# Performance work log

Measured on AMD Instinct MI355X. Metric: run time of the kernel, lower is better.

The kernel has to match this reference:

```python
import jax, jax.numpy as jnp
import numpy as np

H, D = 20, 64  # n_head, head_dim (n_state = 1280)


def setup_inputs() -> dict:
    key = jax.random.key(0)
    ks = jax.random.split(key, 14)
    B, S, N, R = 2, 1500, 1280, 32
    s = 0.05  # keep activations/scores numerically tame
    return {
        "x":   jax.random.normal(ks[0], (B, S, N), jnp.float32),
        "Wq1": jax.random.normal(ks[1], (R, N), jnp.float32) * s,
        "Wq2": jax.random.normal(ks[2], (N, R), jnp.float32) * s,
        "bq":  jax.random.normal(ks[3], (N,), jnp.float32) * s,
        "Wk1": jax.random.normal(ks[4], (R, N), jnp.float32) * s,
        "Wk2": jax.random.normal(ks[5], (N, R), jnp.float32) * s,
        "bk":  jax.random.normal(ks[6], (N,), jnp.float32) * s,
        "Wv1": jax.random.normal(ks[7], (R, N), jnp.float32) * s,
        "Wv2": jax.random.normal(ks[8], (N, R), jnp.float32) * s,
        "bv":  jax.random.normal(ks[9], (N,), jnp.float32) * s,
        "Wo1": jax.random.normal(ks[10], (R, N), jnp.float32) * s,
        "Wo2": jax.random.normal(ks[11], (N, R), jnp.float32) * s,
        "bo":  jax.random.normal(ks[12], (N,), jnp.float32) * s,
    }


def reference(x, Wq1, Wq2, bq, Wk1, Wk2, bk, Wv1, Wv2, bv, Wo1, Wo2, bo):
    B, S, N = x.shape
    # rank-r projections (the only full-size GEMMs over x)
    q1 = x @ Wq1.T  # (B,S,rq)
    k1 = x @ Wk1.T  # (B,S,rk)
    v1 = x @ Wv1.T  # (B,S,rv)
    # per-head factors, matching prepare_custom_kernel()
    Wq2h = Wq2.reshape(H, D, -1).transpose(0, 2, 1)  # (H,rq,D)
    Wk2h = Wk2.reshape(H, D, -1)                     # (H,D,rk)
    Wv2h = Wv2.reshape(H, D, -1).transpose(0, 2, 1)  # (H,rv,D)
    Wm = Wq2h @ Wk2h                                  # (H,rq,rk)
    bqh = bq.reshape(H, 1, D)                         # (H,1,D)
    bkh = bk.reshape(H, 1, D).transpose(0, 2, 1)      # (H,D,1)
    b1 = (Wq2h @ bkh)[:, :, 0]                        # (H,rq)
    b2 = (bqh @ Wk2h)[:, 0, :]                        # (H,rk)
    b3 = (bqh @ bkh)[:, 0, 0]                         # (H,)
    # merged low-rank attention scores: (q1 Wq2 + bq)(Wk2^T k1^T + bk)
    scores = jnp.einsum('bir,hrt,bjt->bhij', q1, Wm, k1)
    scores = scores + jnp.einsum('bir,hr->bhi', q1, b1)[:, :, :, None]
    scores = scores + jnp.einsum('bjt,ht->bhj', k1, b2)[:, :, None, :]
    scores = scores + b3[None, :, None, None]
    attn = jax.nn.softmax(scores * (D ** -0.5), axis=-1)  # SDPA default scale
    Vh = jnp.einsum('bjr,hrd->bhjd', v1, Wv2h)            # (B,H,S,D)
    a = jnp.einsum('bhij,bhjd->bhid', attn, Vh)           # (B,H,S,D)
    wv = a.transpose(0, 2, 1, 3).reshape(B, S, H * D) + bv
    # out projection (also low-rank)
    return (wv @ Wo1.T) @ Wo2.T + bo
```

## Files before the change

### kernel.cpp

```cpp
#include <hip/hip_runtime.h>
#include <math.h>

#define Bb 2
#define Ss 1500
#define SP 1536
#define Nn 1280
#define Hh 20
#define Rr 32
#define NT 24

#define LOG2E 1.44269504088896f

typedef __attribute__((ext_vector_type(8))) short short8;
typedef __attribute__((ext_vector_type(4))) float f32x4;
typedef unsigned short ushort_t;

__device__ __forceinline__ unsigned short f2bf(float f) {
  unsigned u = __float_as_uint(f);
  u += 0x7fffu + ((u >> 16) & 1u);
  return (unsigned short)(u >> 16);
}
__device__ __forceinline__ float bf2f(unsigned short u) {
  return __uint_as_float((unsigned)u << 16);
}
__device__ __forceinline__ unsigned cvtpk(float a, float b) {
  unsigned d;
  asm("v_cvt_pk_bf16_f32 %0, %1, %2" : "=v"(d) : "v"(a), "v"(b));
  return d;
}
__device__ __forceinline__ float fexp2(float x) {
  float r;
  asm("v_exp_f32 %0, %1" : "=v"(r) : "v"(x));
  return r;
}

__device__ __forceinline__ void gload16(const void* g, void* l) {
  __builtin_amdgcn_global_load_lds((const __attribute__((address_space(1))) unsigned int*)g,
                                   (__attribute__((address_space(3))) unsigned int*)l, 16, 0, 0);
}
__device__ __forceinline__ void gload4(const void* g, void* l) {
  __builtin_amdgcn_global_load_lds((const __attribute__((address_space(1))) unsigned int*)g,
                                   (__attribute__((address_space(3))) unsigned int*)l, 4, 0, 0);
}

#define BAR()                                  \
  do {                                         \
    asm volatile("" ::: "memory");             \
    __builtin_amdgcn_s_barrier();              \
    asm volatile("" ::: "memory");             \
  } while (0)

#define VMW(n) asm volatile("s_waitcnt vmcnt(" #n ")" ::: "memory")


__global__ void prep_kernel(const float* __restrict__ x, const float* __restrict__ Wq1,
                            const float* __restrict__ Wk1, const float* __restrict__ Wv1,
                            const float* __restrict__ Wo1, const float* __restrict__ Wq2,
                            const float* __restrict__ Wk2, const float* __restrict__ Wv2,
                            const float* __restrict__ bq, ushort_t* __restrict__ xb,
                            ushort_t* __restrict__ wcatb, ushort_t* __restrict__ wo1b,
                            ushort_t* __restrict__ wv2b, float* __restrict__ wm,
                            float* __restrict__ b2s) {
  int bid = blockIdx.x, tid = threadIdx.x;
  __shared__ float q2s[2048], k2s[2048], bqs[64];
  if (bid < 1920) {
    int gid = bid * 256 + tid;
    int gr = gid / 160, c8 = gid % 160;
    int b = gr / SP, i = gr - b * SP;
    short8 v = (short8){0, 0, 0, 0, 0, 0, 0, 0};
    if (i < Ss) {
      const float* src = x + ((size_t)(b * Ss + i)) * 1280 + c8 * 8;
      float4 a0 = *(const float4*)src;
      float4 a1 = *(const float4*)(src + 4);
      v[0] = (short)f2bf(a0.x); v[1] = (short)f2bf(a0.y);
      v[2] = (short)f2bf(a0.z); v[3] = (short)f2bf(a0.w);
      v[4] = (short)f2bf(a1.x); v[5] = (short)f2bf(a1.y);
      v[6] = (short)f2bf(a1.z); v[7] = (short)f2bf(a1.w);
    }
    *(short8*)(xb + (size_t)gr * 1280 + c8 * 8) = v;
  } else if (bid < 2060) {
    int gid = (bid - 1920) * 256 + tid;
    const float* src = nullptr;
    ushort_t* dst = nullptr;
    if (gid < 20480) {
      int row = gid / 160, c8 = gid % 160;
      dst = wcatb + (size_t)row * 1280 + c8 * 8;
      if (row < 32) src = Wq1 + (size_t)row * 1280 + c8 * 8;
      else if (row < 64) src = Wk1 + (size_t)(row - 32) * 1280 + c8 * 8;
      else if (row < 96) src = Wv1 + (size_t)(row - 64) * 1280 + c8 * 8;
    } else if (gid < 30720) {
      int g = gid - 20480;
      int row = g / 160, c8 = g % 160;
      dst = wo1b + (size_t)row * 1280 + c8 * 8;
      if (row < 32) src = Wo1 + (size_t)row * 1280 + c8 * 8;
    } else {
      int g = gid - 30720;
      int row = g >> 2, c8 = g & 3;
      dst = wv2b + row * 32 + c8 * 8;
      src = Wv2 + row * 32 + c8 * 8;
    }
    short8 v = (short8){0, 0, 0, 0, 0, 0, 0, 0};
    if (src) {
      #pragma unroll
      for (int j = 0; j < 8; ++j) v[j] = (short)f2bf(src[j]);
    }
    *(short8*)dst = v;
  } else {
    int h = bid - 2060;
    for (int e = tid; e < 2048; e += 256) {
      q2s[e] = Wq2[h * 2048 + e];
      k2s[e] = Wk2[h * 2048 + e];
    }
    if (tid < 64) bqs[tid] = bq[h * 64 + tid];
    __syncthreads();
    for (int e = tid; e < 1024; e += 256) {
      int r = e >> 5, t = e & 31;
      float s = 0.f;
      #pragma unroll 16
      for (int d = 0; d < 64; ++d) s += q2s[d * 32 + r] * k2s[d * 32 + t];
      wm[h * 1024 + r * 32 + t] = s * (0.125f * LOG2E);
    }
    if (tid < 32) {
      float s = 0.f;
      #pragma unroll 16
      for (int d = 0; d < 64; ++d) s += bqs[d] * k2s[d * 32 + tid];
      b2s[h * 32 + tid] = s * (0.125f * LOG2E);
    }
  }
}

__global__ __launch_bounds__(128) void gemm_qkv_kernel(
    const ushort_t* __restrict__ xbg, const ushort_t* __restrict__ wcat,
    float* __restrict__ xpq, ushort_t* __restrict__ k1b, ushort_t* __restrict__ v1b) {
  int tid = threadIdx.x, w = tid >> 6, l = tid & 63, l15 = l & 15, l4 = l >> 4;
  int row0 = blockIdx.x * 32;
  __shared__ __align__(16) short As[2][2048];
  __shared__ __align__(16) short Bs[2][6144];
  int sw8 = (((l & 7) ^ ((l >> 3) & 7)) << 3);
  const ushort_t* asrc0 = xbg + (size_t)(row0 + w * 16 + (l >> 3)) * 1280 + sw8;
  const ushort_t* asrc1 = asrc0 + (size_t)8 * 1280;
  const ushort_t* bsrc[6];
  #pragma unroll
  for (int g = 0; g < 6; ++g)
    bsrc[g] = wcat + (size_t)(w * 48 + g * 8 + (l >> 3)) * 1280 + sw8;

#define QSTAGE(bufi, kk)                                            \
  do {                                                              \
    gload16(asrc0 + (kk), &As[bufi][w * 1024]);                     \
    gload16(asrc1 + (kk), &As[bufi][w * 1024 + 512]);               \
    gload16(bsrc[0] + (kk), &Bs[bufi][w * 3072]);                   \
    gload16(bsrc[1] + (kk), &Bs[bufi][w * 3072 + 512]);             \
    gload16(bsrc[2] + (kk), &Bs[bufi][w * 3072 + 1024]);            \
    gload16(bsrc[3] + (kk), &Bs[bufi][w * 3072 + 1536]);            \
    gload16(bsrc[4] + (kk), &Bs[bufi][w * 3072 + 2048]);            \
    gload16(bsrc[5] + (kk), &Bs[bufi][w * 3072 + 2560]);            \
  } while (0)

  f32x4 acc[6];
  #pragma unroll
  for (int nf = 0; nf < 6; ++nf) acc[nf] = (f32x4){0.f, 0.f, 0.f, 0.f};

  QSTAGE(0, 0);
  int cur = 0;
  for (int t = 0; t < 20; ++t) {
    if (t < 19) {
      QSTAGE(cur ^ 1, (t + 1) * 64);
      VMW(8);
    } else {
      VMW(0);
    }
    BAR();
    #pragma unroll
    for (int ks = 0; ks < 2; ++ks) {
      short8 af = *(const short8*)&As[cur][(w * 16 + l15) * 64 +
                                           (((ks * 4 + l4) ^ (l15 & 7)) << 3)];
      #pragma unroll
      for (int nf = 0; nf < 6; ++nf) {
        short8 bf = *(const short8*)&Bs[cur][(nf * 16 + l15) * 64 +
                                             (((ks * 4 + l4) ^ (l15 & 7)) << 3)];
        acc[nf] = __builtin_amdgcn_mfma_f32_16x16x32_bf16(af, bf, acc[nf], 0, 0, 0);
      }
    }
    BAR();
    cur ^= 1;
  }
#undef QSTAGE

  #pragma unroll
  for (int nf = 0; nf < 6; ++nf) {
    int o = nf * 16 + l15;
    #pragma unroll
    for (int reg = 0; reg < 4; ++reg) {
      int gr = row0 + w * 16 + l4 * 4 + reg;
      int b = (gr >= SP) ? 1 : 0;
      int i = gr - b * SP;
      if (i < Ss) {
        float v = acc[nf][reg];
        if (o < 32) xpq[((size_t)b * Ss + i) * 32 + o] = v;
        else if (o < 64) k1b[((size_t)b * SP + i) * 32 + (o - 32)] = f2bf(v);
        else v1b[((size_t)b * 32 + (o - 64)) * SP + i] = f2bf(v);
      }
    }
  }
}

__global__ void qh_kb_kernel(const float* __restrict__ xpq, const float* __restrict__ wm,
                             const float* __restrict__ b2s, const ushort_t* __restrict__ k1b,
                             ushort_t* __restrict__ qhb, float* __restrict__ kbp) {
  int tid = threadIdx.x, b = blockIdx.z;
  if (blockIdx.y == 20) {
    int j0 = blockIdx.x * 64;
    __shared__ float k1s[64 * 33];
    __shared__ float b2sh[20 * 33];
    for (int e = tid; e < 2048; e += 256) {
      int row = e >> 5, t = e & 31;
      k1s[row * 33 + t] = bf2f(k1b[((size_t)b * SP + j0 + row) * 32 + t]);
    }
    for (int e = tid; e < 640; e += 256) b2sh[(e >> 5) * 33 + (e & 31)] = b2s[e];
    __syncthreads();
    for (int e = tid; e < 1280; e += 256) {
      int h = e >> 6, rw = e & 63;
      int j = j0 + rw;
      float s = -1e30f;
      if (j < Ss) {
        s = 0.f;
        #pragma unroll 8
        for (int t = 0; t < 32; ++t) s += k1s[rw * 33 + t] * b2sh[h * 33 + t];
      }
      kbp[((size_t)b * Hh + h) * SP + j] = s;
    }
  } else {
    int it = blockIdx.x, h = blockIdx.y;
    int i0 = it * 64;
    __shared__ float q1s[64 * 33];
    __shared__ float wms[1024];
    for (int e = tid; e < 2048; e += 256) {
      int row = e >> 5, r = e & 31;
      int i = i0 + row;
      q1s[row * 33 + r] = (i < Ss) ? xpq[((size_t)b * Ss + i) * 32 + r] : 0.f;
    }
    for (int e = tid; e < 1024; e += 256) wms[e] = wm[h * 1024 + e];
    __syncthreads();
    int row = tid >> 2, tc = (tid & 3) * 8;
    float o[8];
    #pragma unroll
    for (int j = 0; j < 8; ++j) o[j] = 0.f;
    for (int r = 0; r < 32; ++r) {
      float qv = q1s[row * 33 + r];
      #pragma unroll
      for (int j = 0; j < 8; ++j) o[j] += qv * wms[r * 32 + tc + j];
    }
    short8 sv;
    #pragma unroll
    for (int j = 0; j < 8; ++j) sv[j] = (short)f2bf(o[j]);
    *(short8*)(qhb + ((size_t)(b * Hh + h) * SP + i0 + row) * 32 + tc) = sv;
  }
}

__global__ __launch_bounds__(512) void attn2_kernel(
    const ushort_t* __restrict__ qhg, const ushort_t* __restrict__ k1g,
    const ushort_t* __restrict__ v1g, const ushort_t* __restrict__ wv2g,
    const float* __restrict__ kbg, const float* __restrict__ bv, ushort_t* __restrict__ wvb) {
  int it = blockIdx.x, h = blockIdx.y, b = blockIdx.z;
  int bh = b * Hh + h;
  int i0 = it * 128;
  int tid = threadIdx.x, w = tid >> 6, l = tid & 63;
  int l15 = l & 15, l4 = l >> 4;

  __shared__ short kS[3][2048];
  __shared__ short vS[3][2048];
  __shared__ float kbS[3][64];
  __shared__ short pS[8][1024];
  __shared__ short p2S[8][512];

  short8 qa = *(const short8*)(qhg + ((size_t)bh * SP + i0 + w * 16 + l15) * 32 + l4 * 8);
  short8 wb0 = *(const short8*)(wv2g + (size_t)(h * 64 + 0 * 16 + l15) * 32 + l4 * 8);
  short8 wb1 = *(const short8*)(wv2g + (size_t)(h * 64 + 1 * 16 + l15) * 32 + l4 * 8);
  short8 wb2 = *(const short8*)(wv2g + (size_t)(h * 64 + 2 * 16 + l15) * 32 + l4 * 8);
  short8 wb3 = *(const short8*)(wv2g + (size_t)(h * 64 + 3 * 16 + l15) * 32 + l4 * 8);
  VMW(0);

  const ushort_t* ksrc = k1g + (size_t)b * SP * 32 + l * 32 + (w & 3) * 8;
  const ushort_t* vsrc = v1g + ((size_t)b * 32 + (w & 3) * 8 + (l >> 3)) * SP +
                         (((l & 7) ^ ((l >> 3) & 7)) << 3);
  const float* kbsrc = kbg + (size_t)bh * SP + l;

#define STAGE(bufi, tt)                                         \
  do {                                                          \
    if (w < 4) {                                                \
      int j0s = (tt) * 64;                                      \
      gload16(ksrc + (size_t)j0s * 32, &kS[bufi][w * 512]);     \
      gload16(vsrc + j0s, &vS[bufi][w * 512]);                  \
      if (w == 0) gload4(kbsrc + j0s, &kbS[bufi][0]);           \
    }                                                           \
  } while (0)

  STAGE(0, 0);
  STAGE(1, 1);

  f32x4 pv1[2];
  pv1[0] = (f32x4){0.f, 0.f, 0.f, 0.f};
  pv1[1] = (f32x4){0.f, 0.f, 0.f, 0.f};
  float psr[4] = {0.f, 0.f, 0.f, 0.f};
  const f32x4 zf = (f32x4){0.f, 0.f, 0.f, 0.f};

  int cur = 0;
  for (int t = 0; t < NT; ++t) {
    if (t < NT - 1) {
      if (w == 0) VMW(3);
      else if (w < 4) VMW(2);
    } else {
      if (w < 4) VMW(0);
    }
    BAR();

    __builtin_amdgcn_s_setprio(1);
    #pragma unroll
    for (int nb = 0; nb < 4; ++nb) {
      short8 kf = *(const short8*)&kS[cur][l4 * 512 + (nb * 16 + l15) * 8];
      f32x4 c = __builtin_amdgcn_mfma_f32_16x16x32_bf16(qa, kf, zf, 0, 0, 0);
      float kbv = kbS[cur][nb * 16 + l15];
      int slot_lo = nb * 2 + (l15 >> 3);
      #pragma unroll
      for (int reg = 0; reg < 4; ++reg) {
        int q = l4 * 4 + reg;
        float p = fexp2(c[reg] + kbv);
        psr[reg] += p;
        pS[w][q * 64 + ((slot_lo ^ (q & 7)) << 3) + (l15 & 7)] = (short)cvtpk(p, p);
      }
    }

    #pragma unroll
    for (int kh = 0; kh < 2; ++kh) {
      short8 pa = *(const short8*)&pS[w][l15 * 64 + (((kh * 4 + l4) ^ (l15 & 7)) << 3)];
      #pragma unroll
      for (int nf = 0; nf < 2; ++nf) {
        short8 vf =
            *(const short8*)&vS[cur][(nf * 16 + l15) * 64 + (((kh * 4 + l4) ^ (l15 & 7)) << 3)];
        pv1[nf] = __builtin_amdgcn_mfma_f32_16x16x32_bf16(pa, vf, pv1[nf], 0, 0, 0);
      }
    }
    __builtin_amdgcn_s_setprio(0);

    if (t + 2 < NT) {
      int sb = (cur + 2 >= 3) ? cur - 1 : cur + 2;
      STAGE(sb, t + 2);
    }
    cur = (cur == 2) ? 0 : cur + 1;
  }
#undef STAGE

  #pragma unroll
  for (int nf = 0; nf < 2; ++nf) {
    #pragma unroll
    for (int reg = 0; reg < 4; ++reg) {
      int q = l4 * 4 + reg;
      int slot = nf * 2 + (l15 >> 3);
      p2S[w][q * 32 + ((slot ^ ((q >> 1) & 3)) << 3) + (l15 & 7)] =
          (short)cvtpk(pv1[nf][reg], pv1[nf][reg]);
    }
  }
  short8 pa2 = *(const short8*)&p2S[w][l15 * 32 + ((l4 ^ ((l15 >> 1) & 3)) << 3)];

  f32x4 acc[4];
  acc[0] = __builtin_amdgcn_mfma_f32_16x16x32_bf16(pa2, wb0, zf, 0, 0, 0);
  acc[1] = __builtin_amdgcn_mfma_f32_16x16x32_bf16(pa2, wb1, zf, 0, 0, 0);
  acc[2] = __builtin_amdgcn_mfma_f32_16x16x32_bf16(pa2, wb2, zf, 0, 0, 0);
  acc[3] = __builtin_amdgcn_mfma_f32_16x16x32_bf16(pa2, wb3, zf, 0, 0, 0);

  #pragma unroll
  for (int reg = 0; reg < 4; ++reg) {
    #pragma unroll
    for (int m = 1; m < 16; m <<= 1) psr[reg] += __shfl_xor(psr[reg], m, 64);
  }
  float inv[4];
  #pragma unroll
  for (int reg = 0; reg < 4; ++reg) inv[reg] = 1.f / psr[reg];

  #pragma unroll
  for (int db = 0; db < 4; ++db) {
    float bvv = bv[h * 64 + db * 16 + l15];
    #pragma unroll
    for (int reg = 0; reg < 4; ++reg) {
      int qi = i0 + w * 16 + l4 * 4 + reg;
      if (qi < Ss)
        wvb[((size_t)(b * SP + qi)) * 1280 + h * 64 + db * 16 + l15] =
            f2bf(acc[db][reg] * inv[reg] + bvv);
    }
  }
}

__global__ __launch_bounds__(128) void gemm_o1_kernel(const ushort_t* __restrict__ wvg,
                                                      const ushort_t* __restrict__ wo1,
                                                      float* __restrict__ tbuf) {
  int tid = threadIdx.x, w = tid >> 6, l = tid & 63, l15 = l & 15, l4 = l >> 4;
  int row0 = blockIdx.x * 32;
  __shared__ __align__(16) short As[2][2048];
  __shared__ __align__(16) short Bs[2][2048];
  int sw8 = (((l & 7) ^ ((l >> 3) & 7)) << 3);
  const ushort_t* asrc0 = wvg + (size_t)(row0 + w * 16 + (l >> 3)) * 1280 + sw8;
  const ushort_t* asrc1 = asrc0 + (size_t)8 * 1280;
  const ushort_t* bsrc = wo1 + (size_t)(w * 16 + (l >> 3)) * 1280 + sw8;
  const ushort_t* bsrc1 = bsrc + (size_t)8 * 1280;

#define OSTAGE(bufi, kk)                                 \
  do {                                                   \
    gload16(asrc0 + (kk), &As[bufi][w * 1024]);          \
    gload16(asrc1 + (kk), &As[bufi][w * 1024 + 512]);    \
    gload16(bsrc + (kk), &Bs[bufi][w * 1024]);           \
    gload16(bsrc1 + (kk), &Bs[bufi][w * 1024 + 512]);    \
  } while (0)

  f32x4 acc[2];
  acc[0] = (f32x4){0.f, 0.f, 0.f, 0.f};
  acc[1] = (f32x4){0.f, 0.f, 0.f, 0.f};
  OSTAGE(0, 0);
  int cur = 0;
  for (int t = 0; t < 20; ++t) {
    if (t < 19) {
      OSTAGE(cur ^ 1, (t + 1) * 64);
      VMW(4);
    } else {
      VMW(0);
    }
    BAR();
    #pragma unroll
    for (int ks = 0; ks < 2; ++ks) {
      short8 af = *(const short8*)&As[cur][(w * 16 + l15) * 64 +
                                           (((ks * 4 + l4) ^ (l15 & 7)) << 3)];
      #pragma unroll
      for (int nf = 0; nf < 2; ++nf) {
        short8 bf = *(const short8*)&Bs[cur][(nf * 16 + l15) * 64 +
                                             (((ks * 4 + l4) ^ (l15 & 7)) << 3)];
        acc[nf] = __builtin_amdgcn_mfma_f32_16x16x32_bf16(af, bf, acc[nf], 0, 0, 0);
      }
    }
    BAR();
    cur ^= 1;
  }
#undef OSTAGE

  #pragma unroll
  for (int nf = 0; nf < 2; ++nf) {
    int o = nf * 16 + l15;
    #pragma unroll
    for (int reg = 0; reg < 4; ++reg) {
      int gr = row0 + w * 16 + l4 * 4 + reg;
      int b = (gr >= SP) ? 1 : 0;
      int i = gr - b * SP;
      if (i < Ss) tbuf[((size_t)b * Ss + i) * 32 + o] = acc[nf][reg];
    }
  }
}

__global__ void proj_o2_kernel(const float* __restrict__ tbuf, const float* __restrict__ Wo2,
                               const float* __restrict__ bo, float* __restrict__ out) {
  int rb = blockIdx.x, nb = blockIdx.y, tid = threadIdx.x;
  int rowbase = rb * 16, n0 = nb * 256;
  __shared__ float ts[16 * 33];
  __shared__ float wos[256 * 33];
  for (int e = tid; e < 8192; e += 256) {
    int nloc = e >> 5, o = e & 31;
    wos[nloc * 33 + o] = Wo2[(size_t)(n0 + nloc) * 32 + o];
  }
  for (int e = tid; e < 512; e += 256) {
    int row = e >> 5, o = e & 31;
    int gr = rowbase + row;
    ts[row * 33 + o] = (gr < Bb * Ss) ? tbuf[(size_t)gr * 32 + o] : 0.f;
  }
  __syncthreads();
  int n = n0 + tid;
  float bias = bo[n];
  for (int row = 0; row < 16; ++row) {
    int gr = rowbase + row;
    if (gr >= Bb * Ss) break;
    float s = bias;
    #pragma unroll 8
    for (int o = 0; o < 32; ++o) s += ts[row * 33 + o] * wos[tid * 33 + o];
    out[(size_t)gr * 1280 + n] = s;
  }
}

extern "C" void kernel_launch(void* const* d_in, const int* in_sizes, int n_in,
                              void* d_out, int out_size, void* d_ws, size_t ws_size,
                              hipStream_t stream) {
  const float* x   = (const float*)d_in[0];
  const float* Wq1 = (const float*)d_in[1];
  const float* Wq2 = (const float*)d_in[2];
  const float* bq  = (const float*)d_in[3];
  const float* Wk1 = (const float*)d_in[4];
  const float* Wk2 = (const float*)d_in[5];
  const float* Wv1 = (const float*)d_in[7];
  const float* Wv2 = (const float*)d_in[8];
  const float* bv  = (const float*)d_in[9];
  const float* Wo1 = (const float*)d_in[10];
  const float* Wo2 = (const float*)d_in[11];
  const float* bo  = (const float*)d_in[12];
  float* out = (float*)d_out;
  float* ws  = (float*)d_ws;

  if (ws_size < (size_t)5431424 * sizeof(float)) return;

  float* wm    = ws;
  float* b2s   = ws + 20480;
  float* xpq   = ws + 21120;
  float* kb    = ws + 117120;
  float* tbuf  = ws + 178560;
  ushort_t* qhb   = (ushort_t*)(ws + 274560);
  ushort_t* k1b   = (ushort_t*)(ws + 1257600);
  ushort_t* v1b   = (ushort_t*)(ws + 1306752);
  ushort_t* xb    = (ushort_t*)(ws + 1355904);
  ushort_t* wcatb = (ushort_t*)(ws + 3321984);
  ushort_t* wo1b  = (ushort_t*)(ws + 3403904);
  ushort_t* wv2b  = (ushort_t*)(ws + 3444864);
  ushort_t* wvb   = (ushort_t*)(ws + 3465344);

  prep_kernel<<<2080, 256, 0, stream>>>(x, Wq1, Wk1, Wv1, Wo1, Wq2, Wk2, Wv2, bq,
                                        xb, wcatb, wo1b, wv2b, wm, b2s);
  gemm_qkv_kernel<<<96, 128, 0, stream>>>(xb, wcatb, xpq, k1b, v1b);
  qh_kb_kernel<<<dim3(NT, 21, Bb), 256, 0, stream>>>(xpq, wm, b2s, k1b, qhb, kb);
  attn2_kernel<<<dim3(12, Hh, Bb), 512, 0, stream>>>(qhb, k1b, v1b, wv2b, kb, bv, wvb);
  gemm_o1_kernel<<<96, 128, 0, stream>>>(wvb, wo1b, tbuf);
  proj_o2_kernel<<<dim3(188, 5), 256, 0, stream>>>(tbuf, Wo2, bo, out);
}
```

Measured before the change: 99.18 us.

## Fold key bias term into QKV GEMM as extra weight rows

Precomputes per-head vectors Wk1^T·b2 in prep and appends them as 20 extra rows of the concatenated weight, so the QKV GEMM directly produces the per-key bias kb. This removes the separate kb branch of the qh/kb kernel, and the padding rows of kb are filled with -1e30 in prep. q1 is now stored as bf16 instead of fp32. The GEMM tile grows from 96 to 128 output columns, which adds MFMA work and LDS, and kb now comes from a bf16 GEMM, which loses some precision.

New measurement: 101.6 us. 2.5% more time.

```diff
diff --git a/kernel.cpp b/kernel.cpp
--- a/kernel.cpp
+++ b/kernel.cpp
@@ -60,9 +60,10 @@
                             const float* __restrict__ bq, ushort_t* __restrict__ xb,
                             ushort_t* __restrict__ wcatb, ushort_t* __restrict__ wo1b,
                             ushort_t* __restrict__ wv2b, float* __restrict__ wm,
-                            float* __restrict__ b2s) {
+                            float* __restrict__ b2s, float* __restrict__ kbp) {
   int bid = blockIdx.x, tid = threadIdx.x;
   __shared__ float q2s[2048], k2s[2048], bqs[64];
+  __shared__ float b2sh[32];
   if (bid < 1920) {
     int gid = bid * 256 + tid;
     int gr = gid / 160, c8 = gid % 160;
@@ -84,10 +85,12 @@
     ushort_t* dst = nullptr;
     if (gid < 20480) {
       int row = gid / 160, c8 = gid % 160;
-      dst = wcatb + (size_t)row * 1280 + c8 * 8;
-      if (row < 32) src = Wq1 + (size_t)row * 1280 + c8 * 8;
-      else if (row < 64) src = Wk1 + (size_t)(row - 32) * 1280 + c8 * 8;
-      else if (row < 96) src = Wv1 + (size_t)(row - 64) * 1280 + c8 * 8;
+      if (row < 96 || row >= 116) {
+        dst = wcatb + (size_t)row * 1280 + c8 * 8;
+        if (row < 32) src = Wq1 + (size_t)row * 1280 + c8 * 8;
+        else if (row < 64) src = Wk1 + (size_t)(row - 32) * 1280 + c8 * 8;
+        else if (row < 96) src = Wv1 + (size_t)(row - 64) * 1280 + c8 * 8;
+      }
     } else if (gid < 30720) {
       int g = gid - 20480;
       int row = g / 160, c8 = g % 160;
@@ -99,13 +102,15 @@
       dst = wv2b + row * 32 + c8 * 8;
       src = Wv2 + row * 32 + c8 * 8;
     }
-    short8 v = (short8){0, 0, 0, 0, 0, 0, 0, 0};
-    if (src) {
-      #pragma unroll
-      for (int j = 0; j < 8; ++j) v[j] = (short)f2bf(src[j]);
-    }
-    *(short8*)dst = v;
-  } else {
+    if (dst) {
+      short8 v = (short8){0, 0, 0, 0, 0, 0, 0, 0};
+      if (src) {
+        #pragma unroll
+        for (int j = 0; j < 8; ++j) v[j] = (short)f2bf(src[j]);
+      }
+      *(short8*)dst = v;
+    }
+  } else if (bid < 2080) {
     int h = bid - 2060;
     for (int e = tid; e < 2048; e += 256) {
       q2s[e] = Wq2[h * 2048 + e];
@@ -126,46 +131,71 @@
       for (int d = 0; d < 64; ++d) s += bqs[d] * k2s[d * 32 + tid];
       b2s[h * 32 + tid] = s * (0.125f * LOG2E);
     }
+  } else if (bid < 2180) {
+    int idx = bid - 2080;
+    int h = idx / 5, n = (idx % 5) * 256 + tid;
+    if (tid < 64) bqs[tid] = bq[h * 64 + tid];
+    __syncthreads();
+    if (tid < 32) {
+      float s = 0.f;
+      #pragma unroll 16
+      for (int d = 0; d < 64; ++d) s += bqs[d] * Wk2[(h * 64 + d) * 32 + tid];
+      b2sh[tid] = s * (0.125f * LOG2E);
+    }
+    __syncthreads();
+    float u = 0.f;
+    #pragma unroll 8
+    for (int t = 0; t < 32; ++t) u += b2sh[t] * Wk1[t * 1280 + n];
+    wcatb[(size_t)(96 + h) * 1280 + n] = f2bf(u);
+  } else {
+    for (int e = tid; e < 1440; e += 256) {
+      int b2 = e / 720, rem = e % 720;
+      int h = rem / 36, j = 1500 + rem % 36;
+      kbp[((size_t)b2 * Hh + h) * SP + j] = -1e30f;
+    }
   }
 }
 
 __global__ __launch_bounds__(128) void gemm_qkv_kernel(
     const ushort_t* __restrict__ xbg, const ushort_t* __restrict__ wcat,
-    float* __restrict__ xpq, ushort_t* __restrict__ k1b, ushort_t* __restrict__ v1b) {
+    ushort_t* __restrict__ q1b, ushort_t* __restrict__ k1b, ushort_t* __restrict__ v1b,
+    float* __restrict__ kbp) {
   int tid = threadIdx.x, w = tid >> 6, l = tid & 63, l15 = l & 15, l4 = l >> 4;
   int row0 = blockIdx.x * 32;
   __shared__ __align__(16) short As[2][2048];
-  __shared__ __align__(16) short Bs[2][6144];
+  __shared__ __align__(16) short Bs[2][8192];
   int sw8 = (((l & 7) ^ ((l >> 3) & 7)) << 3);
   const ushort_t* asrc0 = xbg + (size_t)(row0 + w * 16 + (l >> 3)) * 1280 + sw8;
   const ushort_t* asrc1 = asrc0 + (size_t)8 * 1280;
-  const ushort_t* bsrc[6];
-  #pragma unroll
-  for (int g = 0; g < 6; ++g)
-    bsrc[g] = wcat + (size_t)(w * 48 + g * 8 + (l >> 3)) * 1280 + sw8;
+  const ushort_t* bsrc[8];
+  #pragma unroll
+  for (int g = 0; g < 8; ++g)
+    bsrc[g] = wcat + (size_t)(w * 64 + g * 8 + (l >> 3)) * 1280 + sw8;
 
 #define QSTAGE(bufi, kk)                                            \
   do {                                                              \
     gload16(asrc0 + (kk), &As[bufi][w * 1024]);                     \
     gload16(asrc1 + (kk), &As[bufi][w * 1024 + 512]);               \
-    gload16(bsrc[0] + (kk), &Bs[bufi][w * 3072]);                   \
-    gload16(bsrc[1] + (kk), &Bs[bufi][w * 3072 + 512]);             \
-    gload16(bsrc[2] + (kk), &Bs[bufi][w * 3072 + 1024]);            \
-    gload16(bsrc[3] + (kk), &Bs[bufi][w * 3072 + 1536]);            \
-    gload16(bsrc[4] + (kk), &Bs[bufi][w * 3072 + 2048]);            \
-    gload16(bsrc[5] + (kk), &Bs[bufi][w * 3072 + 2560]);            \
+    gload16(bsrc[0] + (kk), &Bs[bufi][w * 4096]);                   \
+    gload16(bsrc[1] + (kk), &Bs[bufi][w * 4096 + 512]);             \
+    gload16(bsrc[2] + (kk), &Bs[bufi][w * 4096 + 1024]);            \
+    gload16(bsrc[3] + (kk), &Bs[bufi][w * 4096 + 1536]);            \
+    gload16(bsrc[4] + (kk), &Bs[bufi][w * 4096 + 2048]);            \
+    gload16(bsrc[5] + (kk), &Bs[bufi][w * 4096 + 2560]);            \
+    gload16(bsrc[6] + (kk), &Bs[bufi][w * 4096 + 3072]);            \
+    gload16(bsrc[7] + (kk), &Bs[bufi][w * 4096 + 3584]);            \
   } while (0)
 
-  f32x4 acc[6];
-  #pragma unroll
-  for (int nf = 0; nf < 6; ++nf) acc[nf] = (f32x4){0.f, 0.f, 0.f, 0.f};
+  f32x4 acc[8];
+  #pragma unroll
+  for (int nf = 0; nf < 8; ++nf) acc[nf] = (f32x4){0.f, 0.f, 0.f, 0.f};
 
   QSTAGE(0, 0);
   int cur = 0;
   for (int t = 0; t < 20; ++t) {
     if (t < 19) {
       QSTAGE(cur ^ 1, (t + 1) * 64);
-      VMW(8);
+      VMW(10);
     } else {
       VMW(0);
     }
@@ -175,7 +205,7 @@
       short8 af = *(const short8*)&As[cur][(w * 16 + l15) * 64 +
                                            (((ks * 4 + l4) ^ (l15 & 7)) << 3)];
       #pragma unroll
-      for (int nf = 0; nf < 6; ++nf) {
+      for (int nf = 0; nf < 8; ++nf) {
         short8 bf = *(const short8*)&Bs[cur][(nf * 16 + l15) * 64 +
                                              (((ks * 4 + l4) ^ (l15 & 7)) << 3)];
         acc[nf] = __builtin_amdgcn_mfma_f32_16x16x32_bf16(af, bf, acc[nf], 0, 0, 0);
@@ -187,7 +217,7 @@
 #undef QSTAGE
 
   #pragma unroll
-  for (int nf = 0; nf < 6; ++nf) {
+  for (int nf = 0; nf < 8; ++nf) {
     int o = nf * 16 + l15;
     #pragma unroll
     for (int reg = 0; reg < 4; ++reg) {
@@ -196,65 +226,41 @@
       int i = gr - b * SP;
       if (i < Ss) {
         float v = acc[nf][reg];
-        if (o < 32) xpq[((size_t)b * Ss + i) * 32 + o] = v;
+        if (o < 32) q1b[((size_t)b * SP + i) * 32 + o] = f2bf(v);
         else if (o < 64) k1b[((size_t)b * SP + i) * 32 + (o - 32)] = f2bf(v);
-        else v1b[((size_t)b * 32 + (o - 64)) * SP + i] = f2bf(v);
-      }
-    }
-  }
-}
-
-__global__ void qh_kb_kernel(const float* __restrict__ xpq, const float* __restrict__ wm,
-                             const float* __restrict__ b2s, const ushort_t* __restrict__ k1b,
-                             ushort_t* __restrict__ qhb, float* __restrict__ kbp) {
-  int tid = threadIdx.x, b = blockIdx.z;
-  if (blockIdx.y == 20) {
-    int j0 = blockIdx.x * 64;
-    __shared__ float k1s[64 * 33];
-    __shared__ float b2sh[20 * 33];
-    for (int e = tid; e < 2048; e += 256) {
-      int row = e >> 5, t = e & 31;
-      k1s[row * 33 + t] = bf2f(k1b[((size_t)b * SP + j0 + row) * 32 + t]);
-    }
-    for (int e = tid; e < 640; e += 256) b2sh[(e >> 5) * 33 + (e & 31)] = b2s[e];
-    __syncthreads();
-    for (int e = tid; e < 1280; e += 256) {
-      int h = e >> 6, rw = e & 63;
-      int j = j0 + rw;
-      float s = -1e30f;
-      if (j < Ss) {
-        s = 0.f;
-        #pragma unroll 8
-        for (int t = 0; t < 32; ++t) s += k1s[rw * 33 + t] * b2sh[h * 33 + t];
-      }
-      kbp[((size_t)b * Hh + h) * SP + j] = s;
-    }
-  } else {
-    int it = blockIdx.x, h = blockIdx.y;
-    int i0 = it * 64;
-    __shared__ float q1s[64 * 33];
-    __shared__ float wms[1024];
-    for (int e = tid; e < 2048; e += 256) {
-      int row = e >> 5, r = e & 31;
-      int i = i0 + row;
-      q1s[row * 33 + r] = (i < Ss) ? xpq[((size_t)b * Ss + i) * 32 + r] : 0.f;
-    }
-    for (int e = tid; e < 1024; e += 256) wms[e] = wm[h * 1024 + e];
-    __syncthreads();
-    int row = tid >> 2, tc = (tid & 3) * 8;
-    float o[8];
-    #pragma unroll
-    for (int j = 0; j < 8; ++j) o[j] = 0.f;
-    for (int r = 0; r < 32; ++r) {
-      float qv = q1s[row * 33 + r];
-      #pragma unroll
-      for (int j = 0; j < 8; ++j) o[j] += qv * wms[r * 32 + tc + j];
-    }
-    short8 sv;
-    #pragma unroll
-    for (int j = 0; j < 8; ++j) sv[j] = (short)f2bf(o[j]);
-    *(short8*)(qhb + ((size_t)(b * Hh + h) * SP + i0 + row) * 32 + tc) = sv;
-  }
+        else if (o < 96) v1b[((size_t)b * 32 + (o - 64)) * SP + i] = f2bf(v);
+        else if (o < 116) kbp[((size_t)b * Hh + (o - 96)) * SP + i] = v;
+      }
+    }
+  }
+}
+
+__global__ void qh_kernel(const ushort_t* __restrict__ q1b, const float* __restrict__ wm,
+                          ushort_t* __restrict__ qhb) {
+  int it = blockIdx.x, h = blockIdx.y, b = blockIdx.z;
+  int i0 = it * 64, tid = threadIdx.x;
+  __shared__ float q1s[64 * 33];
+  __shared__ float wms[1024];
+  for (int e = tid; e < 2048; e += 256) {
+    int row = e >> 5, r = e & 31;
+    int i = i0 + row;
+    q1s[row * 33 + r] = (i < Ss) ? bf2f(q1b[((size_t)b * SP + i) * 32 + r]) : 0.f;
+  }
+  for (int e = tid; e < 1024; e += 256) wms[e] = wm[h * 1024 + e];
+  __syncthreads();
+  int row = tid >> 2, tc = (tid & 3) * 8;
+  float o[8];
+  #pragma unroll
+  for (int j = 0; j < 8; ++j) o[j] = 0.f;
+  for (int r = 0; r < 32; ++r) {
+    float qv = q1s[row * 33 + r];
+    #pragma unroll
+    for (int j = 0; j < 8; ++j) o[j] += qv * wms[r * 32 + tc + j];
+  }
+  short8 sv;
+  #pragma unroll
+  for (int j = 0; j < 8; ++j) sv[j] = (short)f2bf(o[j]);
+  *(short8*)(qhb + ((size_t)(b * Hh + h) * SP + i0 + row) * 32 + tc) = sv;
 }
 
 __global__ __launch_bounds__(512) void attn2_kernel(
@@ -499,27 +505,27 @@
   float* out = (float*)d_out;
   float* ws  = (float*)d_ws;
 
-  if (ws_size < (size_t)5431424 * sizeof(float)) return;
-
-  float* wm    = ws;
-  float* b2s   = ws + 20480;
-  float* xpq   = ws + 21120;
-  float* kb    = ws + 117120;
-  float* tbuf  = ws + 178560;
-  ushort_t* qhb   = (ushort_t*)(ws + 274560);
-  ushort_t* k1b   = (ushort_t*)(ws + 1257600);
-  ushort_t* v1b   = (ushort_t*)(ws + 1306752);
-  ushort_t* xb    = (ushort_t*)(ws + 1355904);
-  ushort_t* wcatb = (ushort_t*)(ws + 3321984);
-  ushort_t* wo1b  = (ushort_t*)(ws + 3403904);
-  ushort_t* wv2b  = (ushort_t*)(ws + 3444864);
-  ushort_t* wvb   = (ushort_t*)(ws + 3465344);
-
-  prep_kernel<<<2080, 256, 0, stream>>>(x, Wq1, Wk1, Wv1, Wo1, Wq2, Wk2, Wv2, bq,
-                                        xb, wcatb, wo1b, wv2b, wm, b2s);
-  gemm_qkv_kernel<<<96, 128, 0, stream>>>(xb, wcatb, xpq, k1b, v1b);
-  qh_kb_kernel<<<dim3(NT, 21, Bb), 256, 0, stream>>>(xpq, wm, b2s, k1b, qhb, kb);
-  attn2_kernel<<<dim3(12, Hh, Bb), 512, 0, stream>>>(qhb, k1b, v1b, wv2b, kb, bv, wvb);
+  if (ws_size < (size_t)5384576 * sizeof(float)) return;
+
+  float* kbp  = ws;
+  float* tbuf = ws + 61440;
+  ushort_t* q1b   = (ushort_t*)(ws + 157440);
+  ushort_t* k1b   = (ushort_t*)(ws + 206592);
+  ushort_t* v1b   = (ushort_t*)(ws + 255744);
+  ushort_t* xb    = (ushort_t*)(ws + 304896);
+  ushort_t* wcatb = (ushort_t*)(ws + 2270976);
+  ushort_t* wo1b  = (ushort_t*)(ws + 2352896);
+  ushort_t* wv2b  = (ushort_t*)(ws + 2393856);
+  float* wm   = ws + 2414336;
+  float* b2s  = ws + 2434816;
+  ushort_t* qhb   = (ushort_t*)(ws + 2435456);
+  ushort_t* wvb   = (ushort_t*)(ws + 3418496);
+
+  prep_kernel<<<2181, 256, 0, stream>>>(x, Wq1, Wk1, Wv1, Wo1, Wq2, Wk2, Wv2, bq,
+                                        xb, wcatb, wo1b, wv2b, wm, b2s, kbp);
+  gemm_qkv_kernel<<<96, 128, 0, stream>>>(xb, wcatb, q1b, k1b, v1b, kbp);
+  qh_kernel<<<dim3(NT, Hh, Bb), 256, 0, stream>>>(q1b, wm, qhb);
+  attn2_kernel<<<dim3(12, Hh, Bb), 512, 0, stream>>>(qhb, k1b, v1b, wv2b, kbp, bv, wvb);
   gemm_o1_kernel<<<96, 128, 0, stream>>>(wvb, wo1b, tbuf);
   proj_o2_kernel<<<dim3(188, 5), 256, 0, stream>>>(tbuf, Wo2, bo, out);
 }
```
